# Performance work log

Hardware: AMD Instinct MI355X
Metric: run time of the kernel (lower is better)

The kernel has to match this reference:

```python
import jax, jax.numpy as jnp
import numpy as np

SIGMAS = jnp.array([0.0001, 0.001, 0.01, 0.1, 1, 5, 10, 15, 20, 25, 30, 100], dtype=jnp.float32)


def setup_inputs() -> dict:
    key = jax.random.key(0)
    k1, k2 = jax.random.split(key)
    N, D = 4096, 256
    feature = jax.random.normal(k1, (N, D), dtype=jnp.float32)
    domain = jax.random.randint(k2, (N,), 0, 8, dtype=jnp.int64)
    return {"feature": feature, "domain": domain}


def reference(feature, domain):
    # Pairwise squared L2 distances via the Gram trick (avoids NxNxD intermediate).
    sq = jnp.sum(feature * feature, axis=1)            # [N]
    gram = feature @ feature.T                          # [N, N]
    d2 = jnp.maximum(sq[:, None] + sq[None, :] - 2.0 * gram, 0.0)  # [N, N]

    # Multi-sigma Gaussian kernel sum: sum_s exp(-d2/2 * s). Loop over the
    # small fixed set of 12 sigmas to avoid a 12xNxN intermediate.
    k = jnp.zeros_like(d2)
    for s in [0.0001, 0.001, 0.01, 0.1, 1.0, 5.0, 10.0, 15.0, 20.0, 25.0, 30.0, 100.0]:
        k = k + jnp.exp(-d2 * (0.5 * s))

    same = (domain[:, None] == domain[None, :]).astype(jnp.float32)  # [N, N]
    neg = 1.0 - same
    Ex = jnp.sum(same * k) / jnp.sum(same)
    Ey = jnp.sum(neg * k) / jnp.sum(neg)
    return Ex - Ey
```

## Files before the change

kernel.cpp:

```cpp
#include <hip/hip_runtime.h>


typedef __attribute__((ext_vector_type(8))) short short8;
typedef __attribute__((ext_vector_type(4))) float floatx4;

#define AS1 __attribute__((address_space(1)))
#define AS3 __attribute__((address_space(3)))

__device__ inline unsigned f2bf2(float lo, float hi) {
  union { float f; unsigned u; } a, b; a.f = lo; b.f = hi;
  unsigned ra = (a.u + 0x7fffu + ((a.u >> 16) & 1u)) >> 16;
  unsigned rb = (b.u + 0x7fffu + ((b.u >> 16) & 1u)) >> 16;
  return ra | (rb << 16);
}

__device__ inline float fast_exp2(float x) {
#if __has_builtin(__builtin_amdgcn_exp2f)
  return __builtin_amdgcn_exp2f(x);
#else
  return exp2f(x);
#endif
}

__global__ __launch_bounds__(256) void prep_kernel(
    const float* __restrict__ feat, uint4* __restrict__ fbt,
    float* __restrict__ sqpart, int N, int D) {
  const int tid = threadIdx.x;
  const int rt = blockIdx.x >> 2;
  const int kq = blockIdx.x & 3;
  const int r = tid & 63;
  const int nkc = D >> 3;
  __shared__ float sqp[256];
  float ss = 0.f;
  #pragma unroll
  for (int it = 0; it < 2; ++it) {
    const int kc = kq * 8 + it * 4 + (tid >> 6);
    const float4* src = (const float4*)(feat + (size_t)(rt * 64 + r) * D + kc * 8);
    float4 v0 = src[0], v1 = src[1];
    ss += v0.x*v0.x + v0.y*v0.y + v0.z*v0.z + v0.w*v0.w
        + v1.x*v1.x + v1.y*v1.y + v1.z*v1.z + v1.w*v1.w;
    uint4 o;
    o.x = f2bf2(v0.x, v0.y); o.y = f2bf2(v0.z, v0.w);
    o.z = f2bf2(v1.x, v1.y); o.w = f2bf2(v1.z, v1.w);
    fbt[(size_t)rt * nkc * 64 + kc * 64 + r] = o;
  }
  sqp[tid] = ss;
  __syncthreads();
  if (tid < 64)
    sqpart[(size_t)kq * N + rt * 64 + tid] =
        sqp[tid] + sqp[tid + 64] + sqp[tid + 128] + sqp[tid + 192];
}

__global__ __launch_bounds__(512, 4) void mmd_main(
    const uint4* __restrict__ fbt, const float* __restrict__ sqpart,
    const int* __restrict__ dom, float2* __restrict__ partial, int N) {
  int b = blockIdx.x;
  int i = (int)((sqrtf(8.f * (float)b + 1.f) - 1.f) * 0.5f);
  while ((i + 1) * (i + 2) / 2 <= b) ++i;
  while (i * (i + 1) / 2 > b) --i;
  const int ti = b - i * (i + 1) / 2;
  const int tj = i;
  const int rowI = ti * 128, rowJ = tj * 128;

  __shared__ __align__(16) uint4 Bs[4096];
  __shared__ float sqI[128], sqJ[128];
  __shared__ int dmI[128], dmJ[128];
  __shared__ float red[16];

  const int tid = threadIdx.x;
  const int lane = tid & 63, w = tid >> 6;
  const int quad = lane >> 4, m16 = lane & 15;

  const uint4* At = fbt + (size_t)ti * 4096;
  const uint4* Bt = fbt + (size_t)tj * 4096;

  #pragma unroll
  for (int p = 0; p < 8; ++p) {
    const int base = p * 512 + w * 64;
#if __has_builtin(__builtin_amdgcn_global_load_lds)
    __builtin_amdgcn_global_load_lds(
        (const AS1 uint4*)(Bt + base + lane),
        (AS3 uint4*)(Bs + base), 16, 0, 0);
#else
    Bs[base + lane] = Bt[base + lane];
#endif
  }

  short8 afrag[8];
  {
    const uint4* Aw = At + (size_t)(w >> 2) * 2048 + (w & 3) * 16 + m16;
    #pragma unroll
    for (int s = 0; s < 8; ++s) {
      uint4 t = Aw[(s * 4 + quad) * 64];
      afrag[s] = *(short8*)&t;
    }
  }

  if (tid < 128) {
    sqI[tid] = sqpart[rowI + tid] + sqpart[N + rowI + tid]
             + sqpart[2 * N + rowI + tid] + sqpart[3 * N + rowI + tid];
    dmI[tid] = dom[rowI + tid];
  } else if (tid < 256) {
    int t = tid - 128;
    sqJ[t] = sqpart[rowJ + t] + sqpart[N + rowJ + t]
           + sqpart[2 * N + rowJ + t] + sqpart[3 * N + rowJ + t];
    dmJ[t] = dom[rowJ + t];
  }
  __syncthreads();

  floatx4 acc[8];
  #pragma unroll
  for (int t = 0; t < 8; ++t) acc[t] = (floatx4){0.f, 0.f, 0.f, 0.f};

  #pragma unroll
  for (int s = 0; s < 8; ++s) {
    #pragma unroll
    for (int t = 0; t < 8; ++t) {
      const uint4* bp = Bs + (size_t)(t >> 2) * 2048
                      + (s * 4 + quad) * 64 + (t & 3) * 16 + m16;
      uint4 bt = *bp;
      acc[t] = __builtin_amdgcn_mfma_f32_16x16x32_bf16(
                   afrag[s], *(short8*)&bt, acc[t], 0, 0, 0);
    }
  }

  const float C0 = -7.2134752e-05f, C1 = -7.2134752e-04f, C2 = -7.2134752e-03f,
              C3 = -7.2134752e-02f, C4 = -0.72134752f, C5 = -3.6067376f,
              C100 = -72.13475204f;

  float s_all = 0.f, s_same = 0.f;
  const int r0 = w * 16 + quad * 4;
  float sqr[4]; int dmr[4];
  #pragma unroll
  for (int reg = 0; reg < 4; ++reg) { sqr[reg] = sqI[r0 + reg]; dmr[reg] = dmI[r0 + reg]; }

  #pragma unroll
  for (int t = 0; t < 8; ++t) {
    const int c = t * 16 + m16;
    const float sqc = sqJ[c];
    const int dc = dmJ[c];
    const int gj = rowJ + c;
    #pragma unroll
    for (int reg = 0; reg < 4; ++reg) {
      const int gi = rowI + r0 + reg;
      float d2 = sqr[reg] + sqc - 2.f * acc[t][reg];
      d2 = fmaxf(d2, 0.f);
      if (gi == gj) d2 = 0.f;
      float e0 = fast_exp2(d2 * C0), e1 = fast_exp2(d2 * C1);
      float e2 = fast_exp2(d2 * C2), e3 = fast_exp2(d2 * C3);
      float e4 = fast_exp2(d2 * C4), e5 = fast_exp2(d2 * C5);
      float e11 = fast_exp2(d2 * C100);
      float t10 = e5 * e5, t15 = t10 * e5, t20 = t10 * t10;
      float t25 = t15 * t10, t30 = t15 * t15;
      float kk = ((e0 + e1) + (e2 + e3)) + ((e4 + e5) + (t10 + t15))
               + ((t20 + t25) + (t30 + e11));
      s_all += kk;
      if (dmr[reg] == dc) s_same += kk;
    }
  }
  #pragma unroll
  for (int off = 32; off > 0; off >>= 1) {
    s_all  += __shfl_down(s_all, off);
    s_same += __shfl_down(s_same, off);
  }
  if (lane == 0) { red[w] = s_all; red[8 + w] = s_same; }
  __syncthreads();
  if (tid == 0) {
    const float wt = (ti == tj) ? 1.f : 2.f;
    float a = 0.f, s = 0.f;
    #pragma unroll
    for (int k = 0; k < 8; ++k) { a += red[k]; s += red[8 + k]; }
    partial[b] = make_float2(s * wt, a * wt);
  }
}

__global__ __launch_bounds__(256) void finalize_kernel(
    const float2* __restrict__ partial, int nblk,
    const int* __restrict__ dom, float* __restrict__ out, int N) {
  __shared__ int histL[16];
  __shared__ double redS[8];
  const int tid = threadIdx.x;
  if (tid < 16) histL[tid] = 0;
  __syncthreads();
  for (int i = tid; i < N; i += 256) atomicAdd(&histL[dom[i] & 15], 1);
  double as = 0.0, aa = 0.0;
  for (int i = tid; i < nblk; i += 256) {
    float2 p = partial[i];
    as += (double)p.x; aa += (double)p.y;
  }
  #pragma unroll
  for (int off = 32; off > 0; off >>= 1) {
    as += __shfl_down(as, off);
    aa += __shfl_down(aa, off);
  }
  const int w = tid >> 6;
  if ((tid & 63) == 0) { redS[w] = as; redS[4 + w] = aa; }
  __syncthreads();
  if (tid == 0) {
    double S = redS[0] + redS[1] + redS[2] + redS[3];
    double A = redS[4] + redS[5] + redS[6] + redS[7];
    double csame = 0.0;
    for (int i = 0; i < 16; ++i) { double h = (double)histL[i]; csame += h * h; }
    double call = (double)N * (double)N;
    out[0] = (float)(S / csame - (A - S) / (call - csame));
  }
}

extern "C" void kernel_launch(void* const* d_in, const int* in_sizes, int n_in,
                              void* d_out, int out_size, void* d_ws, size_t ws_size,
                              hipStream_t stream) {
  const float* feat = (const float*)d_in[0];
  const int* dom = (const int*)d_in[1];
  float* out = (float*)d_out;
  const int N = in_sizes[1];
  const int D = in_sizes[0] / N;
  const int T = N / 128;
  const int nblk = T * (T + 1) / 2;

  char* ws = (char*)d_ws;
  float2* partial = (float2*)ws;
  float* sqpart = (float*)(ws + 16640);
  uint4* fbt = (uint4*)(ws + 82176);

  prep_kernel<<<dim3((N / 64) * 4), dim3(256), 0, stream>>>(feat, fbt, sqpart, N, D);
  mmd_main<<<dim3(nblk), dim3(512), 0, stream>>>(fbt, sqpart, dom, partial, N);
  finalize_kernel<<<1, 256, 0, stream>>>(partial, nblk, dom, out, N);
}
```

Measured before the change: 83.53 us.

## Fuse finalize into main kernel, interleave MFMA with exp, skip small-kernel exps

Folds the single-block finalize kernel into the main kernel: the last block to finish, found with an atomic counter reset in the prep kernel, does the final reduction. This removes one launch. The MFMA loop is reordered so each 16-column tile is computed and then consumed right away, which cuts the live accumulator registers from 32 to 4 and mixes matrix work with exp work. The exps for the larger sigmas are skipped when d2 is large enough that they underflow to zero. The risks are divergence in the skipped branch and a last-block sync that depends on correct fences.

```diff
diff --git a/kernel.cpp b/kernel.cpp
--- a/kernel.cpp
+++ b/kernel.cpp
@@ -24,8 +24,9 @@
 
 __global__ __launch_bounds__(256) void prep_kernel(
     const float* __restrict__ feat, uint4* __restrict__ fbt,
-    float* __restrict__ sqpart, int N, int D) {
+    float* __restrict__ sqpart, unsigned* __restrict__ counter, int N, int D) {
   const int tid = threadIdx.x;
+  if (blockIdx.x == 0 && tid == 0) *counter = 0u;
   const int rt = blockIdx.x >> 2;
   const int kq = blockIdx.x & 3;
   const int r = tid & 63;
@@ -53,7 +54,16 @@
 
 __global__ __launch_bounds__(512, 4) void mmd_main(
     const uint4* __restrict__ fbt, const float* __restrict__ sqpart,
-    const int* __restrict__ dom, float2* __restrict__ partial, int N) {
+    const int* __restrict__ dom, float2* __restrict__ partial,
+    unsigned* __restrict__ counter, float* __restrict__ out, int N) {
+  __shared__ __align__(16) uint4 Bs[4096];
+  __shared__ float sqI[128], sqJ[128];
+  __shared__ int dmI[128], dmJ[128];
+  __shared__ float red[16];
+  __shared__ double redD[16];
+  __shared__ int histL[16];
+  __shared__ int lastFlag;
+
   int b = blockIdx.x;
   int i = (int)((sqrtf(8.f * (float)b + 1.f) - 1.f) * 0.5f);
   while ((i + 1) * (i + 2) / 2 <= b) ++i;
@@ -61,11 +71,6 @@
   const int ti = b - i * (i + 1) / 2;
   const int tj = i;
   const int rowI = ti * 128, rowJ = tj * 128;
-
-  __shared__ __align__(16) uint4 Bs[4096];
-  __shared__ float sqI[128], sqJ[128];
-  __shared__ int dmI[128], dmJ[128];
-  __shared__ float red[16];
 
   const int tid = threadIdx.x;
   const int lane = tid & 63, w = tid >> 6;
@@ -108,52 +113,41 @@
   }
   __syncthreads();
 
-  floatx4 acc[8];
-  #pragma unroll
-  for (int t = 0; t < 8; ++t) acc[t] = (floatx4){0.f, 0.f, 0.f, 0.f};
-
-  #pragma unroll
-  for (int s = 0; s < 8; ++s) {
-    #pragma unroll
-    for (int t = 0; t < 8; ++t) {
-      const uint4* bp = Bs + (size_t)(t >> 2) * 2048
-                      + (s * 4 + quad) * 64 + (t & 3) * 16 + m16;
-      uint4 bt = *bp;
-      acc[t] = __builtin_amdgcn_mfma_f32_16x16x32_bf16(
-                   afrag[s], *(short8*)&bt, acc[t], 0, 0, 0);
-    }
-  }
-
   const float C0 = -7.2134752e-05f, C1 = -7.2134752e-04f, C2 = -7.2134752e-03f,
               C3 = -7.2134752e-02f, C4 = -0.72134752f, C5 = -3.6067376f,
               C100 = -72.13475204f;
 
-  float s_all = 0.f, s_same = 0.f;
   const int r0 = w * 16 + quad * 4;
   float sqr[4]; int dmr[4];
   #pragma unroll
   for (int reg = 0; reg < 4; ++reg) { sqr[reg] = sqI[r0 + reg]; dmr[reg] = dmI[r0 + reg]; }
 
+  float s_all = 0.f, s_same = 0.f;
   #pragma unroll
   for (int t = 0; t < 8; ++t) {
+    floatx4 acc = (floatx4){0.f, 0.f, 0.f, 0.f};
+    const uint4* bp = Bs + (size_t)(t >> 2) * 2048 + quad * 64 + (t & 3) * 16 + m16;
+    #pragma unroll
+    for (int s = 0; s < 8; ++s) {
+      uint4 bt = bp[s * 256];
+      acc = __builtin_amdgcn_mfma_f32_16x16x32_bf16(afrag[s], *(short8*)&bt, acc, 0, 0, 0);
+    }
     const int c = t * 16 + m16;
     const float sqc = sqJ[c];
     const int dc = dmJ[c];
-    const int gj = rowJ + c;
     #pragma unroll
     for (int reg = 0; reg < 4; ++reg) {
-      const int gi = rowI + r0 + reg;
-      float d2 = sqr[reg] + sqc - 2.f * acc[t][reg];
-      d2 = fmaxf(d2, 0.f);
-      if (gi == gj) d2 = 0.f;
-      float e0 = fast_exp2(d2 * C0), e1 = fast_exp2(d2 * C1);
-      float e2 = fast_exp2(d2 * C2), e3 = fast_exp2(d2 * C3);
-      float e4 = fast_exp2(d2 * C4), e5 = fast_exp2(d2 * C5);
-      float e11 = fast_exp2(d2 * C100);
-      float t10 = e5 * e5, t15 = t10 * e5, t20 = t10 * t10;
-      float t25 = t15 * t10, t30 = t15 * t15;
-      float kk = ((e0 + e1) + (e2 + e3)) + ((e4 + e5) + (t10 + t15))
-               + ((t20 + t25) + (t30 + e11));
+      float d2 = fmaxf(fmaf(-2.f, acc[reg], sqr[reg] + sqc), 0.f);
+      float kk = fast_exp2(d2 * C0) + fast_exp2(d2 * C1)
+               + fast_exp2(d2 * C2) + fast_exp2(d2 * C3);
+      if (d2 < 176.f) {
+        float e4 = fast_exp2(d2 * C4), e5 = fast_exp2(d2 * C5);
+        float e11 = fast_exp2(d2 * C100);
+        float t10 = e5 * e5, t15 = t10 * e5, t20 = t10 * t10;
+        float t25 = t15 * t10, t30 = t15 * t15;
+        kk += ((e4 + e5) + (t10 + t15)) + ((t20 + t25) + (t30 + e11));
+        if (ti == tj && (r0 + reg) == c) kk = 12.f;
+      }
       s_all += kk;
       if (dmr[reg] == dc) s_same += kk;
     }
@@ -171,36 +165,36 @@
     #pragma unroll
     for (int k = 0; k < 8; ++k) { a += red[k]; s += red[8 + k]; }
     partial[b] = make_float2(s * wt, a * wt);
-  }
-}
-
-__global__ __launch_bounds__(256) void finalize_kernel(
-    const float2* __restrict__ partial, int nblk,
-    const int* __restrict__ dom, float* __restrict__ out, int N) {
-  __shared__ int histL[16];
-  __shared__ double redS[8];
-  const int tid = threadIdx.x;
+    __threadfence();
+    unsigned prev = atomicAdd(counter, 1u);
+    lastFlag = (prev == gridDim.x - 1) ? 1 : 0;
+  }
+  __syncthreads();
+  if (!lastFlag) return;
+
+  __threadfence();
+  const int nblk = gridDim.x;
   if (tid < 16) histL[tid] = 0;
   __syncthreads();
-  for (int i = tid; i < N; i += 256) atomicAdd(&histL[dom[i] & 15], 1);
+  for (int k = tid; k < N; k += 512) atomicAdd(&histL[dom[k] & 15], 1);
   double as = 0.0, aa = 0.0;
-  for (int i = tid; i < nblk; i += 256) {
-    float2 p = partial[i];
-    as += (double)p.x; aa += (double)p.y;
+  for (int k = tid; k < nblk; k += 512) {
+    volatile float2* vp = (volatile float2*)&partial[k];
+    as += (double)vp->x; aa += (double)vp->y;
   }
   #pragma unroll
   for (int off = 32; off > 0; off >>= 1) {
     as += __shfl_down(as, off);
     aa += __shfl_down(aa, off);
   }
-  const int w = tid >> 6;
-  if ((tid & 63) == 0) { redS[w] = as; redS[4 + w] = aa; }
+  if (lane == 0) { redD[w] = as; redD[8 + w] = aa; }
   __syncthreads();
   if (tid == 0) {
-    double S = redS[0] + redS[1] + redS[2] + redS[3];
-    double A = redS[4] + redS[5] + redS[6] + redS[7];
+    double S = 0.0, A = 0.0;
+    #pragma unroll
+    for (int k = 0; k < 8; ++k) { S += redD[k]; A += redD[8 + k]; }
     double csame = 0.0;
-    for (int i = 0; i < 16; ++i) { double h = (double)histL[i]; csame += h * h; }
+    for (int k = 0; k < 16; ++k) { double h = (double)histL[k]; csame += h * h; }
     double call = (double)N * (double)N;
     out[0] = (float)(S / csame - (A - S) / (call - csame));
   }
@@ -219,10 +213,10 @@
 
   char* ws = (char*)d_ws;
   float2* partial = (float2*)ws;
+  unsigned* counter = (unsigned*)(ws + 16384);
   float* sqpart = (float*)(ws + 16640);
   uint4* fbt = (uint4*)(ws + 82176);
 
-  prep_kernel<<<dim3((N / 64) * 4), dim3(256), 0, stream>>>(feat, fbt, sqpart, N, D);
-  mmd_main<<<dim3(nblk), dim3(512), 0, stream>>>(fbt, sqpart, dom, partial, N);
-  finalize_kernel<<<1, 256, 0, stream>>>(partial, nblk, dom, out, N);
-}
+  prep_kernel<<<dim3((N / 64) * 4), dim3(256), 0, stream>>>(feat, fbt, sqpart, counter, N, D);
+  mmd_main<<<dim3(nblk), dim3(512), 0, stream>>>(fbt, sqpart, dom, partial, counter, out, N);
+}
```

Result: slower. 85.68 us (+2.6%).
